# Kernel optimization log

Hardware: AMD Instinct MI355X
Metric: run time of the kernel (lower is better)

The kernel has to match this reference:

```python
import jax, jax.numpy as jnp
import numpy as np
import math

NUM_ITER = 5
FEAT_STRIDE = 16
GAUSS_SIGMA = 1.0
HINGE_THRESHOLD = -999.0
MIN_FILTER_REG = 1e-3
ALPHA_EPS = 0.0


def apply_filter(feat, weights):
    # feat: (ni, ns, C, H, W); weights: (ns, C, fH, fW) -> scores (ni, ns, oH, oW)
    ni, ns, C, H, W = feat.shape
    fH, fW = weights.shape[-2], weights.shape[-1]
    x = feat.reshape(ni, ns * C, H, W)
    out = jax.lax.conv_general_dilated(
        x, weights, window_strides=(1, 1),
        padding=((fH // 2, fH // 2), (fW // 2, fW // 2)),
        dimension_numbers=('NCHW', 'OIHW', 'NCHW'),
        feature_group_count=ns)
    return out  # (ni, ns, oH, oW); oH = H + (fH+1)%2


def get_label(center, out_sz, sigma):
    # center: (ni, ns, 2) in (row, col) order
    k0 = jnp.arange(out_sz[0], dtype=jnp.float32)[None, None, :, None]
    k1 = jnp.arange(out_sz[1], dtype=jnp.float32)[None, None, None, :]
    g0 = jnp.exp(-0.5 / (sigma * sigma) * (k0 - center[..., 0][..., None, None]) ** 2)
    g1 = jnp.exp(-0.5 / (sigma * sigma) * (k1 - center[..., 1][..., None, None]) ** 2)
    return g0 * g1  # (ni, ns, oH, oW)


def _forward(weights, feat, bb, log_step_length, filter_reg):
    ni, ns = feat.shape[0], feat.shape[1]
    fH, fW = weights.shape[-2], weights.shape[-1]
    out_sz = (feat.shape[-2] + (fH + 1) % 2, feat.shape[-1] + (fW + 1) % 2)
    step = jnp.exp(log_step_length)[0]
    reg = jnp.maximum(filter_reg * filter_reg, MIN_FILTER_REG ** 2)[0]
    dmap_offset = jnp.array([fH % 2, fW % 2], jnp.float32) / 2.0
    # (x, y) -> (row, col), feature-grid coordinates
    center = ((bb[..., :2] + bb[..., 2:] / 2.0) / FEAT_STRIDE)[..., ::-1] - dmap_offset
    label = get_label(center, out_sz, GAUSS_SIGMA)
    mask = (label > HINGE_THRESHOLD).astype(feat.dtype)
    label = label * mask
    sw = math.sqrt(1.0 / ni)

    losses = []
    for _ in range(NUM_ITER):
        scores = apply_filter(feat, weights)
        scores_act = mask * scores + (1.0 - mask) * jax.nn.relu(scores)
        score_mask = mask + (1.0 - mask) * (jax.lax.stop_gradient(scores) > 0).astype(scores.dtype)
        residuals = sw * (scores_act - label)
        losses.append((jnp.sum(residuals ** 2) + reg * jnp.sum(weights ** 2)) / ns)
        residuals_mapped = score_mask * (sw * residuals)
        # feat-transpose = adjoint of apply_filter w.r.t. the filter weights
        _, vjp_fn = jax.vjp(lambda w: apply_filter(feat, w), weights)
        data_grad = vjp_fn(residuals_mapped)[0]
        weights_grad = data_grad + reg * weights
        scores_grad = apply_filter(feat, weights_grad)
        scores_grad = sw * (score_mask * scores_grad)
        alpha_num = jnp.sum(weights_grad ** 2, axis=(1, 2, 3))  # (ns,)
        alpha_den = jnp.maximum(
            jnp.sum(scores_grad.reshape(ni, ns, -1) ** 2, axis=(0, 2))
            + (reg + ALPHA_EPS) * alpha_num, 1e-8)
        alpha = alpha_num / alpha_den
        weights = weights - step * alpha[:, None, None, None] * weights_grad

    scores = apply_filter(feat, weights)
    scores = mask * scores + (1.0 - mask) * jax.nn.relu(scores)
    losses.append((jnp.sum((sw * (scores - label)) ** 2) + reg * jnp.sum(weights ** 2)) / ns)
    return weights, jnp.stack(losses)


def setup_inputs() -> dict:
    key = jax.random.key(0)
    k1, k2, k3, k4 = jax.random.split(key, 4)
    ni, ns, C, H, W, fH, fW = 3, 32, 512, 22, 22, 4, 4
    weights = 0.01 * jax.random.normal(k1, (ns, C, fH, fW), jnp.float32)
    feat = jax.random.normal(k2, (ni, ns, C, H, W), jnp.float32)
    # boxes (x, y, w, h) in image coords (image size = 22*16 = 352)
    xy = jax.random.uniform(k3, (ni, ns, 2), jnp.float32, 50.0, 250.0)
    wh = jax.random.uniform(k4, (ni, ns, 2), jnp.float32, 32.0, 96.0)
    bb = jnp.concatenate([xy, wh], axis=-1)
    log_step_length = jnp.zeros((1,), jnp.float32)  # log(1.0)
    filter_reg = 0.01 * jnp.ones((1,), jnp.float32)
    return {"weights": weights, "feat": feat, "bb": bb,
            "log_step_length": log_step_length, "filter_reg": filter_reg}


def reference(weights, feat, bb, log_step_length, filter_reg):
    return _forward(weights, feat, bb, log_step_length, filter_reg)
```

## Files before the change

### kernel.cpp

```cpp
#include <hip/hip_runtime.h>
#include <hip/hip_fp16.h>

#define NI 3
#define NS 32
#define CHN 512
#define OH 23
#define P2 529
#define NP 50784
#define UV 484
#define WSZ 262144
#define KTOT 1536
#define RSP 1544

typedef unsigned int uint32;
typedef unsigned short u16;
typedef _Float16 h2 __attribute__((ext_vector_type(2)));
typedef _Float16 f16x8 __attribute__((ext_vector_type(8)));
typedef float f32x4 __attribute__((ext_vector_type(4)));

#define OFF_FEATT 0UL
#define OFF_LABEL 47579136UL
#define OFF_S0    47782272UL
#define OFF_S1    47985408UL
#define OFF_SGRAW 48188544UL
#define OFF_WG    48391680UL
#define OFF_WGF16 49440256UL
#define OFF_W0F16 49964544UL
#define OFF_PART  50488832UL
#define OFF_FEATC 50521600UL

#define P_DEN   0
#define P_NUM   4320
#define P_LOSS  5600
#define P_WSQ0  5760
#define P_WSQA  5792
#define P_WSQ5  6816
#define P_L5    7840

__device__ __forceinline__ float waveSum(float v) {
#pragma unroll
  for (int o = 32; o > 0; o >>= 1) v += __shfl_xor(v, o, 64);
  return v;
}

__device__ __forceinline__ float alphaFor(const float* __restrict__ part, int t, int s,
                                          float reg) {
  const float* np_ = part + P_NUM + (size_t)(t * NS + s) * 8;
  const float* dp_ = part + P_DEN + (size_t)(t * NS + s) * 6;
  float nu = 0.f;
#pragma unroll
  for (int i = 0; i < 8; ++i) nu += np_[i];
  float de = 0.f;
#pragma unroll
  for (int i = 0; i < 6; ++i) de += dp_[i];
  return nu / fmaxf(de + reg * nu, 1e-8f);
}

__global__ __launch_bounds__(256) void k_setup(const float* __restrict__ feat,
                                               const float* __restrict__ w0,
                                               const float* __restrict__ bb,
                                               u16* __restrict__ featT,
                                               u16* __restrict__ featC,
                                               u16* __restrict__ w0f16,
                                               float* __restrict__ wmaster,
                                               float* __restrict__ label,
                                               float* __restrict__ part) {
  __shared__ uint32 lds32[64 * 121];
  __shared__ float sred[4];
  int b = blockIdx.x, tid = threadIdx.x;
  if (b < 1536) {
    int snT = b >> 4, r4 = b & 15;
    int cb = r4 >> 1, uvh = r4 & 1;
    int s = snT / 3, n = snT % 3;
    const float* fsrc =
        feat + ((size_t)n * NS + s) * CHN * UV + (size_t)(cb * 64) * UV + uvh * 242;
#pragma unroll
    for (int it = 0; it < 31; ++it) {
      int idx = it * 256 + tid;
      if (idx < 7744) {
        int r = (unsigned)idx / 121u;
        int j = idx - r * 121;
        float2 v = *(const float2*)(fsrc + (size_t)r * UV + 2 * j);
        lds32[idx] = (uint32)__half_as_ushort(__float2half(v.x)) |
                     ((uint32)__half_as_ushort(__float2half(v.y)) << 16);
      }
    }
    __syncthreads();
    uint32* dstT = (uint32*)featT +
                   ((size_t)(snT * 4 + (cb >> 1)) * UV + uvh * 242) * 64 + (cb & 1) * 32;
#pragma unroll
    for (int it = 0; it < 31; ++it) {
      int o = it * 256 + tid;
      if (o < 7744) {
        int uv = o >> 5, k = o & 31;
        uint32 wa = lds32[(2 * k) * 121 + (uv >> 1)];
        uint32 wb = lds32[(2 * k + 1) * 121 + (uv >> 1)];
        uint32 h0 = (uv & 1) ? (wa >> 16) : (wa & 0xffffu);
        uint32 h1 = (uv & 1) ? (wb >> 16) : (wb & 0xffffu);
        dstT[(size_t)uv * 64 + k] = h0 | (h1 << 16);
      }
    }
    uint32* dstC =
        (uint32*)featC + ((size_t)(s * CHN + cb * 64)) * 768 + n * 256 + uvh * 121;
    if (uvh == 0) {
#pragma unroll
      for (int it = 0; it < 31; ++it) {
        int idx = it * 256 + tid;
        if (idx < 7744) {
          int c = (unsigned)idx / 121u;
          int j = idx - c * 121;
          dstC[(size_t)c * 768 + j] = lds32[idx];
        }
      }
    } else {
#pragma unroll
      for (int it = 0; it < 34; ++it) {
        int idx = it * 256 + tid;
        if (idx < 8640) {
          int c = (unsigned)idx / 135u;
          int j = idx - c * 135;
          dstC[(size_t)c * 768 + j] = (j < 121) ? lds32[c * 121 + j] : 0u;
        }
      }
    }
  } else if (b < 1568) {
    int s = b - 1536;
    for (int i = tid; i < 8192; i += 256) {
      int tap = i >> 9, c = i & 511;
      w0f16[(size_t)s * 8192 + i] =
          __half_as_ushort(__float2half(w0[(size_t)s * 8192 + c * 16 + tap]));
    }
    float sq = 0.f;
    for (int i = tid; i < 8192; i += 256) {
      float v = w0[(size_t)s * 8192 + i];
      wmaster[(size_t)s * 8192 + i] = v;
      sq += v * v;
    }
    sq = waveSum(sq);
    if ((tid & 63) == 0) sred[tid >> 6] = sq;
    __syncthreads();
    if (tid == 0) part[P_WSQ0 + s] = sred[0] + sred[1] + sred[2] + sred[3];
  } else {
    int p = (b - 1568) * 256 + tid;
    if (p < NP) {
      int nsid = p / P2, rem = p % P2;
      int i = rem / OH, j = rem % OH;
      const float* bp = bb + (size_t)nsid * 4;
      float cr = (bp[1] + 0.5f * bp[3]) * 0.0625f;
      float cc = (bp[0] + 0.5f * bp[2]) * 0.0625f;
      float dy = (float)i - cr, dx = (float)j - cc;
      label[p] = __expf(-0.5f * (dy * dy + dx * dx));
    }
  }
}

__global__ __launch_bounds__(1024) void k_conv_fwd(const u16* __restrict__ featT,
                                                   const u16* __restrict__ wf16,
                                                   float* __restrict__ outbuf, int t,
                                                   float* __restrict__ part) {
  __shared__ uint32 w_lds[16 * 260];
  __shared__ float G[288 * 17];
  __shared__ float dred[16];
  int tid = threadIdx.x;
  int bidx = blockIdx.x;
  int snT = bidx >> 1, h = bidx & 1;
  int s = snT / 3, n = snT - s * 3;
  const uint32* wsrc = (const uint32*)(wf16 + (size_t)s * 8192);
  for (int i = tid; i < 4096; i += 1024) {
    int tap = i >> 8, p = i & 255;
    w_lds[tap * 260 + p] = wsrc[i];
  }
  __syncthreads();
  int wave = tid >> 6, lane = tid & 63;
  int q = lane >> 4, m16 = lane & 15;
  int uv0 = h ? 220 : 0;
  int ntiles = 18 - h;
  int t0 = wave;
  bool has2 = (wave + 16 < ntiles);
  int t1 = has2 ? wave + 16 : wave;
  f32x4 acc0 = {0.f, 0.f, 0.f, 0.f}, acc1 = {0.f, 0.f, 0.f, 0.f};
  size_t base = (size_t)snT * 4 * UV * 128;
  int r0i = uv0 + t0 * 16 + m16;
  if (r0i > 483) r0i = 483;
  int r1i = uv0 + t1 * 16 + m16;
  if (r1i > 483) r1i = 483;
  size_t row0 = (size_t)r0i * 128;
  size_t row1 = (size_t)r1i * 128;
#pragma unroll
  for (int step = 0; step < 16; ++step) {
    int cb = step >> 2, cin = (step & 3) * 32;
    size_t cbase = base + (size_t)cb * UV * 128 + cin + q * 8;
    f16x8 a0 = *(const f16x8*)(featT + cbase + row0);
    uint4 bw = *(const uint4*)&w_lds[m16 * 260 + step * 16 + q * 4];
    f16x8 bf = __builtin_bit_cast(f16x8, bw);
    acc0 = __builtin_amdgcn_mfma_f32_16x16x32_f16(a0, bf, acc0, 0, 0, 0);
    if (has2) {
      f16x8 a1 = *(const f16x8*)(featT + cbase + row1);
      acc1 = __builtin_amdgcn_mfma_f32_16x16x32_f16(a1, bf, acc1, 0, 0, 0);
    }
  }
#pragma unroll
  for (int r = 0; r < 4; ++r) G[(t0 * 16 + q * 4 + r) * 17 + m16] = acc0[r];
  if (has2) {
#pragma unroll
    for (int r = 0; r < 4; ++r) G[(t1 * 16 + q * 4 + r) * 17 + m16] = acc1[r];
  }
  __syncthreads();
  float dsq = 0.f;
  int y0 = h ? 12 : 0;
  int npix = h ? 253 : 276;
  int p = tid;
  if (p < npix) {
    int yl = p / 23, x = p - yl * 23;
    int y = y0 + yl;
    float val = 0.f;
#pragma unroll
    for (int ky = 0; ky < 4; ++ky) {
      int u = y + ky - 2;
      if ((unsigned)u < 22u) {
#pragma unroll
        for (int kx = 0; kx < 4; ++kx) {
          int v = x + kx - 2;
          if ((unsigned)v < 22u) val += G[(u * 22 + v - uv0) * 17 + ky * 4 + kx];
        }
      }
    }
    outbuf[(size_t)(n * NS + s) * P2 + y * 23 + x] = val;
    dsq = val * val;
  }
  if (t >= 0) {
    dsq = waveSum(dsq);
    if (lane == 0) dred[wave] = dsq;
    __syncthreads();
    if (tid == 0) {
      float dsum = 0.f;
#pragma unroll
      for (int i = 0; i < 16; ++i) dsum += dred[i];
      part[P_DEN + ((size_t)(t * NS + s) * 3 + n) * 2 + h] = dsum * (1.0f / 3.0f);
    }
  }
}

__global__ __launch_bounds__(512) void k_adjoint(
    int t, const u16* __restrict__ featC, const float* __restrict__ label,
    const float* __restrict__ scores_old, float* __restrict__ scores_new,
    const float* __restrict__ sgraw, float* __restrict__ wg, u16* __restrict__ wgf16,
    float* __restrict__ wmaster, float* __restrict__ part, const float* __restrict__ lsl,
    const float* __restrict__ fr) {
  __shared__ float r_lds[3 * P2];
  __shared__ __align__(16) u16 rs[16 * RSP];
  __shared__ __align__(16) float kred[4][64][4];
  __shared__ float lred[8], nred8[8], wred8[8];
  int tid = threadIdx.x;
  int s = blockIdx.x >> 3, chunk = blockIdx.x & 7;
  int c0 = chunk * 64;
  float step = __expf(lsl[0]);
  float frv = fr[0];
  float reg = fmaxf(frv * frv, 1e-6f);
  float alpha_p = (t >= 1) ? alphaFor(part, t - 1, s, reg) : 0.f;

  float lsum = 0.f;
  for (int pl = tid; pl < 1587; pl += 512) {
    int nn = (unsigned)pl / (unsigned)P2;
    int rem = pl - nn * P2;
    size_t gp = (size_t)(nn * NS + s) * P2 + rem;
    float S = scores_old[gp];
    if (t >= 1) S -= step * alpha_p * sgraw[gp];
    float d = S - label[gp];
    r_lds[nn * P2 + rem] = d * (1.0f / 3.0f);
    if (chunk == 0) {
      if (t >= 1) scores_new[gp] = S;
      lsum += d * d;
    }
  }
  lsum = waveSum(lsum);
  if ((tid & 63) == 0) lred[tid >> 6] = lsum;
  __syncthreads();
  if (chunk == 0 && tid == 0) {
    float L = 0.f;
#pragma unroll
    for (int i = 0; i < 8; ++i) L += lred[i];
    part[P_LOSS + t * NS + s] = L * (1.0f / 3.0f);
  }

  for (int idx = tid; idx < 16 * RSP; idx += 512) {
    int tap = (unsigned)idx / (unsigned)RSP;
    int k = idx - tap * RSP;
    float val = 0.f;
    if (k < KTOT) {
      int n = k >> 9, uv = k & 511;
      if (uv < UV) {
        int u = (unsigned)uv / 22u;
        int v = uv - u * 22;
        int ky = tap >> 2, kx = tap & 3;
        int y = u + 2 - ky, x = v + 2 - kx;
        if ((unsigned)y < 23u && (unsigned)x < 23u) val = r_lds[n * P2 + y * OH + x];
      }
    }
    rs[idx] = __half_as_ushort(__float2half(val));
  }
  __syncthreads();

  int wave = tid >> 6, lane = tid & 63;
  int q = lane >> 4, m16 = lane & 15;
  int tile = wave & 3, khalf = wave >> 2;
  int c = c0 + tile * 16 + m16;
  const u16* arow = featC + ((size_t)(s * CHN + c)) * KTOT + khalf * 768 + q * 8;
  const u16* brow = rs + m16 * RSP + khalf * 768 + q * 8;
  f32x4 acc = {0.f, 0.f, 0.f, 0.f};
#pragma unroll
  for (int ks = 0; ks < 24; ++ks) {
    f16x8 a = *(const f16x8*)(arow + ks * 32);
    f16x8 bf = *(const f16x8*)(brow + ks * 32);
    acc = __builtin_amdgcn_mfma_f32_16x16x32_f16(a, bf, acc, 0, 0, 0);
  }
  if (khalf == 1) *(f32x4*)&kred[tile][lane][0] = acc;
  __syncthreads();

  float num_part = 0.f, wsq_part = 0.f;
  if (khalf == 0) {
    f32x4 o = *(const f32x4*)&kred[tile][lane][0];
    acc += o;
    int tap = m16;
    int ccb = c0 + tile * 16 + q * 4;
    union { u16 h[4]; uint2 v2; } pk;
#pragma unroll
    for (int r = 0; r < 4; ++r) {
      int cc = ccb + r;
      size_t widx = (size_t)s * 8192 + (size_t)cc * 16 + tap;
      float wold = wmaster[widx];
      float wnew = wold;
      if (t >= 1) {
        wnew = wold - step * alpha_p * wg[widx];
        wmaster[widx] = wnew;
      }
      float wgn = acc[r] + reg * wnew;
      wg[widx] = wgn;
      pk.h[r] = __half_as_ushort(__float2half(wgn));
      wsq_part += wnew * wnew;
      num_part += wgn * wgn;
    }
    *(uint2*)&wgf16[(size_t)s * 8192 + (size_t)tap * 512 + ccb] = pk.v2;
  }
  num_part = waveSum(num_part);
  wsq_part = waveSum(wsq_part);
  if (lane == 0) {
    nred8[wave] = num_part;
    wred8[wave] = wsq_part;
  }
  __syncthreads();
  if (tid == 0) {
    float nsum = 0.f, wsum = 0.f;
#pragma unroll
    for (int i = 0; i < 8; ++i) {
      nsum += nred8[i];
      wsum += wred8[i];
    }
    part[P_NUM + (size_t)(t * NS + s) * 8 + chunk] = nsum;
    if (t >= 1) part[P_WSQA + (size_t)((t - 1) * NS + s) * 8 + chunk] = wsum;
  }
}

__global__ void k_final(float* __restrict__ wmaster, const float* __restrict__ wg,
                        const float* __restrict__ scores4, const float* __restrict__ sgraw,
                        const float* __restrict__ label, float* __restrict__ part,
                        const float* __restrict__ lsl, const float* __restrict__ fr) {
  __shared__ float alpha_s[32];
  __shared__ float red4[4];
  int b = blockIdx.x, tid = threadIdx.x;
  float step = __expf(lsl[0]);
  float frv = fr[0];
  float reg = fmaxf(frv * frv, 1e-6f);
  if (tid < 32) alpha_s[tid] = alphaFor(part, 4, tid, reg);
  __syncthreads();
  if (b < 1024) {
    int idx = b * 256 + tid;
    int s = idx >> 13;
    float w5 = wmaster[idx] - step * alpha_s[s] * wg[idx];
    wmaster[idx] = w5;
    float sq = waveSum(w5 * w5);
    if ((tid & 63) == 0) red4[tid >> 6] = sq;
    __syncthreads();
    if (tid == 0) part[P_WSQ5 + b] = red4[0] + red4[1] + red4[2] + red4[3];
  } else {
    int p = (b - 1024) * 256 + tid;
    float contrib = 0.f;
    if (p < NP) {
      int nsid = p / P2;
      int s = nsid & 31;
      float s5 = scores4[p] - step * alpha_s[s] * sgraw[p];
      float d = s5 - label[p];
      contrib = d * d;
    }
    contrib = waveSum(contrib);
    if ((tid & 63) == 0) red4[tid >> 6] = contrib;
    __syncthreads();
    if (tid == 0)
      part[P_L5 + (b - 1024)] = (red4[0] + red4[1] + red4[2] + red4[3]) * (1.0f / 3.0f);
  }
}

__global__ void k_losses(float* __restrict__ out_losses, const float* __restrict__ part,
                         const float* __restrict__ fr) {
  __shared__ float red[8];
  int tid = threadIdx.x;
  float frv = fr[0];
  float reg = fmaxf(frv * frv, 1e-6f);
  float v5 = 0.f;
  for (int i = tid; i < 1024; i += 256) v5 += part[P_WSQ5 + i];
  v5 = waveSum(v5);
  if ((tid & 63) == 0) red[tid >> 6] = v5;
  __syncthreads();
  float wsq5 = red[0] + red[1] + red[2] + red[3];
  float l5 = 0.f;
  for (int i = tid; i < 199; i += 256) l5 += part[P_L5 + i];
  l5 = waveSum(l5);
  if ((tid & 63) == 0) red[4 + (tid >> 6)] = l5;
  __syncthreads();
  float loss5 = red[4] + red[5] + red[6] + red[7];
  if (tid < 5) {
    int t = tid;
    float ls = 0.f;
    for (int i = 0; i < 32; ++i) ls += part[P_LOSS + t * NS + i];
    float ws_ = 0.f;
    if (t == 0) {
      for (int i = 0; i < 32; ++i) ws_ += part[P_WSQ0 + i];
    } else {
      for (int i = 0; i < 256; ++i) ws_ += part[P_WSQA + (t - 1) * 256 + i];
    }
    out_losses[t] = (ls + reg * ws_) * (1.0f / 32.0f);
  }
  if (tid == 5) out_losses[5] = (loss5 + reg * wsq5) * (1.0f / 32.0f);
}

extern "C" void kernel_launch(void* const* d_in, const int* in_sizes, int n_in,
                              void* d_out, int out_size, void* d_ws, size_t ws_size,
                              hipStream_t stream) {
  const float* w0 = (const float*)d_in[0];
  const float* feat = (const float*)d_in[1];
  const float* bb = (const float*)d_in[2];
  const float* lsl = (const float*)d_in[3];
  const float* fr = (const float*)d_in[4];
  float* out = (float*)d_out;
  char* ws = (char*)d_ws;
  u16* featT = (u16*)(ws + OFF_FEATT);
  float* label = (float*)(ws + OFF_LABEL);
  float* s0 = (float*)(ws + OFF_S0);
  float* s1 = (float*)(ws + OFF_S1);
  float* sgraw = (float*)(ws + OFF_SGRAW);
  float* wg = (float*)(ws + OFF_WG);
  u16* wgf16 = (u16*)(ws + OFF_WGF16);
  u16* w0f16 = (u16*)(ws + OFF_W0F16);
  float* part = (float*)(ws + OFF_PART);
  u16* featC = (u16*)(ws + OFF_FEATC);

  k_setup<<<1767, 256, 0, stream>>>(feat, w0, bb, featT, featC, w0f16, out, label, part);
  k_conv_fwd<<<192, 1024, 0, stream>>>(featT, w0f16, s0, -1, part);
  float* sbuf[2] = {s0, s1};
  for (int t = 0; t < 5; ++t) {
    const float* so = (t == 0) ? s0 : sbuf[(t - 1) & 1];
    float* sn = sbuf[t & 1];
    k_adjoint<<<256, 512, 0, stream>>>(t, featC, label, so, sn, sgraw, wg, wgf16, out, part,
                                       lsl, fr);
    k_conv_fwd<<<192, 1024, 0, stream>>>(featT, wgf16, sgraw, t, part);
  }
  k_final<<<1223, 256, 0, stream>>>(out, wg, s0, sgraw, label, part, lsl, fr);
  k_losses<<<1, 256, 0, stream>>>(out + WSZ, part, fr);
}
```

Measured before the change: 384.1 us.

## Split adjoint K reduction across four wave groups and widen featT transpose stores

The adjoint kernel now launches 1024 threads per block and splits the 1536-long K dimension of its MFMA GEMM into four quarters instead of two. Partial accumulators are combined through a larger LDS buffer, which shortens each wave's serial MFMA chain and adds latency hiding on the global featC loads. Separately, the setup transpose into featT now packs four halves per thread and writes 64-bit stores instead of 32-bit ones, halving the iteration count. The costs are more LDS use, more register pressure from the 1024 launch bound, and a three-way reduction step.

```diff
diff --git a/kernel.cpp b/kernel.cpp
--- a/kernel.cpp
+++ b/kernel.cpp
@@ -89,15 +89,19 @@
     uint32* dstT = (uint32*)featT +
                    ((size_t)(snT * 4 + (cb >> 1)) * UV + uvh * 242) * 64 + (cb & 1) * 32;
 #pragma unroll
-    for (int it = 0; it < 31; ++it) {
+    for (int it = 0; it < 16; ++it) {
       int o = it * 256 + tid;
-      if (o < 7744) {
-        int uv = o >> 5, k = o & 31;
-        uint32 wa = lds32[(2 * k) * 121 + (uv >> 1)];
-        uint32 wb = lds32[(2 * k + 1) * 121 + (uv >> 1)];
-        uint32 h0 = (uv & 1) ? (wa >> 16) : (wa & 0xffffu);
-        uint32 h1 = (uv & 1) ? (wb >> 16) : (wb & 0xffffu);
-        dstT[(size_t)uv * 64 + k] = h0 | (h1 << 16);
+      if (o < 3872) {
+        int uv = o >> 4, kp = o & 15;
+        int j = uv >> 1, sh = (uv & 1) * 16;
+        uint32 a0 = lds32[(4 * kp + 0) * 121 + j];
+        uint32 a1 = lds32[(4 * kp + 1) * 121 + j];
+        uint32 a2 = lds32[(4 * kp + 2) * 121 + j];
+        uint32 a3 = lds32[(4 * kp + 3) * 121 + j];
+        uint2 val;
+        val.x = ((a0 >> sh) & 0xffffu) | (((a1 >> sh) & 0xffffu) << 16);
+        val.y = ((a2 >> sh) & 0xffffu) | (((a3 >> sh) & 0xffffu) << 16);
+        *(uint2*)(dstT + (size_t)uv * 64 + 2 * kp) = val;
       }
     }
     uint32* dstC =
@@ -241,7 +245,7 @@
   }
 }
 
-__global__ __launch_bounds__(512) void k_adjoint(
+__global__ __launch_bounds__(1024) void k_adjoint(
     int t, const u16* __restrict__ featC, const float* __restrict__ label,
     const float* __restrict__ scores_old, float* __restrict__ scores_new,
     const float* __restrict__ sgraw, float* __restrict__ wg, u16* __restrict__ wgf16,
@@ -249,8 +253,8 @@
     const float* __restrict__ fr) {
   __shared__ float r_lds[3 * P2];
   __shared__ __align__(16) u16 rs[16 * RSP];
-  __shared__ __align__(16) float kred[4][64][4];
-  __shared__ float lred[8], nred8[8], wred8[8];
+  __shared__ __align__(16) float kred[3 * 4 * 64 * 4];
+  __shared__ float lred[16], nred[16], wred[16];
   int tid = threadIdx.x;
   int s = blockIdx.x >> 3, chunk = blockIdx.x & 7;
   int c0 = chunk * 64;
@@ -260,7 +264,7 @@
   float alpha_p = (t >= 1) ? alphaFor(part, t - 1, s, reg) : 0.f;
 
   float lsum = 0.f;
-  for (int pl = tid; pl < 1587; pl += 512) {
+  for (int pl = tid; pl < 1587; pl += 1024) {
     int nn = (unsigned)pl / (unsigned)P2;
     int rem = pl - nn * P2;
     size_t gp = (size_t)(nn * NS + s) * P2 + rem;
@@ -279,11 +283,11 @@
   if (chunk == 0 && tid == 0) {
     float L = 0.f;
 #pragma unroll
-    for (int i = 0; i < 8; ++i) L += lred[i];
+    for (int i = 0; i < 16; ++i) L += lred[i];
     part[P_LOSS + t * NS + s] = L * (1.0f / 3.0f);
   }
 
-  for (int idx = tid; idx < 16 * RSP; idx += 512) {
+  for (int idx = tid; idx < 16 * RSP; idx += 1024) {
     int tap = (unsigned)idx / (unsigned)RSP;
     int k = idx - tap * RSP;
     float val = 0.f;
@@ -303,24 +307,25 @@
 
   int wave = tid >> 6, lane = tid & 63;
   int q = lane >> 4, m16 = lane & 15;
-  int tile = wave & 3, khalf = wave >> 2;
+  int tile = wave & 3, kq = wave >> 2;
   int c = c0 + tile * 16 + m16;
-  const u16* arow = featC + ((size_t)(s * CHN + c)) * KTOT + khalf * 768 + q * 8;
-  const u16* brow = rs + m16 * RSP + khalf * 768 + q * 8;
+  const u16* arow = featC + ((size_t)(s * CHN + c)) * KTOT + kq * 384 + q * 8;
+  const u16* brow = rs + m16 * RSP + kq * 384 + q * 8;
   f32x4 acc = {0.f, 0.f, 0.f, 0.f};
 #pragma unroll
-  for (int ks = 0; ks < 24; ++ks) {
+  for (int ks = 0; ks < 12; ++ks) {
     f16x8 a = *(const f16x8*)(arow + ks * 32);
     f16x8 bf = *(const f16x8*)(brow + ks * 32);
     acc = __builtin_amdgcn_mfma_f32_16x16x32_f16(a, bf, acc, 0, 0, 0);
   }
-  if (khalf == 1) *(f32x4*)&kred[tile][lane][0] = acc;
+  if (kq) *(f32x4*)&kred[(((kq - 1) * 4 + tile) * 64 + lane) * 4] = acc;
   __syncthreads();
 
   float num_part = 0.f, wsq_part = 0.f;
-  if (khalf == 0) {
-    f32x4 o = *(const f32x4*)&kred[tile][lane][0];
-    acc += o;
+  if (kq == 0) {
+#pragma unroll
+    for (int kk = 0; kk < 3; ++kk)
+      acc += *(const f32x4*)&kred[((kk * 4 + tile) * 64 + lane) * 4];
     int tap = m16;
     int ccb = c0 + tile * 16 + q * 4;
     union { u16 h[4]; uint2 v2; } pk;
@@ -345,16 +350,16 @@
   num_part = waveSum(num_part);
   wsq_part = waveSum(wsq_part);
   if (lane == 0) {
-    nred8[wave] = num_part;
-    wred8[wave] = wsq_part;
+    nred[wave] = num_part;
+    wred[wave] = wsq_part;
   }
   __syncthreads();
   if (tid == 0) {
     float nsum = 0.f, wsum = 0.f;
 #pragma unroll
-    for (int i = 0; i < 8; ++i) {
-      nsum += nred8[i];
-      wsum += wred8[i];
+    for (int i = 0; i < 16; ++i) {
+      nsum += nred[i];
+      wsum += wred[i];
     }
     part[P_NUM + (size_t)(t * NS + s) * 8 + chunk] = nsum;
     if (t >= 1) part[P_WSQA + (size_t)((t - 1) * NS + s) * 8 + chunk] = wsum;
@@ -460,8 +465,8 @@
   for (int t = 0; t < 5; ++t) {
     const float* so = (t == 0) ? s0 : sbuf[(t - 1) & 1];
     float* sn = sbuf[t & 1];
-    k_adjoint<<<256, 512, 0, stream>>>(t, featC, label, so, sn, sgraw, wg, wgf16, out, part,
-                                       lsl, fr);
+    k_adjoint<<<256, 1024, 0, stream>>>(t, featC, label, so, sn, sgraw, wg, wgf16, out,
+                                        part, lsl, fr);
     k_conv_fwd<<<192, 1024, 0, stream>>>(featT, wgf16, sgraw, t, part);
   }
   k_final<<<1223, 256, 0, stream>>>(out, wg, s0, sgraw, label, part, lsl, fr);
```

After: 370.4 us. 1.04x faster.
